# Kernel tuning notes

Measured on AMD Instinct MI355X. Metric: run time of the kernel, lower is better.

## Reference

```python
import jax, jax.numpy as jnp
import numpy as np

FRONT, END = 1, 2            # COMBINE_FRONT / COMBINE_END label values
BOS_ID, EOS_ID = 0, 1
BS, SLEN, D, H, L = 16, 256, 1024, 16, 2
N_POS = 512                  # N_MAX_POSITIONS


def setup_inputs():
    key = jax.random.key(0)
    ks = iter(jax.random.split(key, 80))
    nrm = lambda shape: jax.random.normal(next(ks), shape, dtype=jnp.float32) * 0.02
    inp = {}
    inp["encoded"] = jax.random.normal(next(ks), (BS, SLEN, D), dtype=jnp.float32)
    inp["lengths"] = jnp.full((BS,), SLEN, dtype=jnp.int32)  # assert slen == lengths.max()
    # deterministic valid word-span labels: [F,F,F,E,O,F,E,O] repeated -> words of 4 and 2 subwords
    pat = np.tile(np.array([1, 1, 1, 2, 0, 1, 2, 0], dtype=np.int32), SLEN // 8)
    inp["combine_labels"] = jnp.asarray(np.broadcast_to(pat, (BS, SLEN)).copy())
    inp["lang_id"] = 0
    inp["pos_emb"] = nrm((N_POS, D))
    inp["special_emb"] = nrm((3, D)).at[2].set(0.0)  # padding_idx=2 row zeroed
    for p in ("ctx", "wc"):
        for w in ("Wq", "Wk", "Wv", "Wo"):
            inp[p + "_" + w] = nrm((L, D, D))
        for b in ("bq", "bk", "bv", "bo", "b2", "be1", "be2"):
            inp[p + "_" + b] = jnp.zeros((L, D), dtype=jnp.float32)
        inp[p + "_W1"] = nrm((L, D, 4 * D))
        inp[p + "_b1"] = jnp.zeros((L, 4 * D), dtype=jnp.float32)
        inp[p + "_W2"] = nrm((L, 4 * D, D))
        inp[p + "_g1"] = jnp.ones((L, D), dtype=jnp.float32)
        inp[p + "_g2"] = jnp.ones((L, D), dtype=jnp.float32)
    return inp


def _ln(x, g, b):
    m = x.mean(-1, keepdims=True)
    v = ((x - m) ** 2).mean(-1, keepdims=True)
    return (x - m) / jnp.sqrt(v + 1e-5) * g + b


def _encoder(x, pad, P):
    # post-norm TransformerEncoder (torch default): attn -> add&LN -> relu-FFN -> add&LN
    Wq, Wk, Wv, Wo, bq, bk, bv, bo, W1, b1, W2, b2, g1, be1, g2, be2 = P
    B, S, Dm = x.shape
    hd = Dm // H
    scale = 1.0 / np.sqrt(hd)
    for i in range(Wq.shape[0]):
        q = (x @ Wq[i] + bq[i]).reshape(B, S, H, hd)
        k = (x @ Wk[i] + bk[i]).reshape(B, S, H, hd)
        v = (x @ Wv[i] + bv[i]).reshape(B, S, H, hd)
        s = jnp.einsum("bqhd,bkhd->bhqk", q, k) * scale
        s = jnp.where(pad[:, None, None, :], -1e9, s)  # src_key_padding_mask
        a = jax.nn.softmax(s, axis=-1)
        o = jnp.einsum("bhqk,bkhd->bqhd", a, v).reshape(B, S, Dm) @ Wo[i] + bo[i]
        x = _ln(x + o, g1[i], be1[i])
        h = jax.nn.relu(x @ W1[i] + b1[i]) @ W2[i] + b2[i]
        x = _ln(x + h, g2[i], be2[i])
    return x


def _word_inputs(encoded, combine_labels, special_emb):
    # vectorized replacement of the nested python-loop ragged span builder;
    # index math on the (concrete) labels in numpy, gathers/scatters in jnp.
    cl = np.asarray(combine_labels)
    f = cl == FRONT
    e = cl == END
    c = np.cumsum(f.astype(np.int64), axis=1)
    frontrun = c - np.maximum.accumulate(np.where(f, 0, c), axis=1)  # run of FRONTs ending here
    fr_prev = np.pad(frontrun[:, :-1], ((0, 0), (1, 0)))
    slot = np.where(f, frontrun, fr_prev + 1)  # 1-based slot inside word (slot 0 = BOS)
    e_flat = e.reshape(-1)
    wid = np.cumsum(e_flat) - e_flat  # word id = #ENDs strictly before, row-major order
    tok_idx = np.nonzero((f | e).reshape(-1))[0]
    w_tok = wid[tok_idx]
    s_tok = slot.reshape(-1)[tok_idx]
    wlen = fr_prev[e] + 3  # k subwords (fr_prev+1) + BOS + EOS
    n_word = wlen.shape[0]
    maxL = int(wlen.max())
    Dm = encoded.shape[-1]
    x = jnp.zeros((n_word, maxL, Dm), dtype=encoded.dtype)
    x = x.at[:, 0].set(special_emb[BOS_ID])
    x = x.at[np.arange(n_word), wlen - 1].set(special_emb[EOS_ID])  # eos at slot k+1
    x = x.at[w_tok, s_tok].set(encoded.reshape(-1, Dm)[tok_idx])
    return x, wlen


def _forward(encoded, lengths, combine_labels, pos_emb, special_emb, ctx, wc):
    S = encoded.shape[1]
    pad = jnp.asarray(np.arange(S)[None, :] >= np.asarray(lengths)[:, None])
    x = _encoder(encoded + pos_emb[:S][None], pad, ctx)          # another_encode
    winp, wlen = _word_inputs(x, combine_labels, special_emb)    # ragged gather, [n_word, maxL, D]
    maxL = winp.shape[1]
    wpad = jnp.asarray(np.arange(maxL)[None, :] >= wlen[:, None])
    y = _encoder(winp + pos_emb[:maxL][None], wpad, wc)          # word_encode
    return y[:, 0]  # position-0 (BOS) representation, [n_word, D]


def reference(encoded, lengths, combine_labels, lang_id, pos_emb, special_emb,
              ctx_Wq, ctx_Wk, ctx_Wv, ctx_Wo, ctx_bq, ctx_bk, ctx_bv, ctx_bo,
              ctx_W1, ctx_b1, ctx_W2, ctx_b2, ctx_g1, ctx_be1, ctx_g2, ctx_be2,
              wc_Wq, wc_Wk, wc_Wv, wc_Wo, wc_bq, wc_bk, wc_bv, wc_bo,
              wc_W1, wc_b1, wc_W2, wc_b2, wc_g1, wc_be1, wc_g2, wc_be2):
    ctx = (ctx_Wq, ctx_Wk, ctx_Wv, ctx_Wo, ctx_bq, ctx_bk, ctx_bv, ctx_bo,
           ctx_W1, ctx_b1, ctx_W2, ctx_b2, ctx_g1, ctx_be1, ctx_g2, ctx_be2)
    wc = (wc_Wq, wc_Wk, wc_Wv, wc_Wo, wc_bq, wc_bk, wc_bv, wc_bo,
          wc_W1, wc_b1, wc_W2, wc_b2, wc_g1, wc_be1, wc_g2, wc_be2)
    return _forward(encoded, lengths, combine_labels, pos_emb, special_emb, ctx, wc)
```

## Files before the change

### kernel.cpp

```cpp
#include <hip/hip_runtime.h>
#include <stdint.h>

typedef unsigned short u16;
typedef __attribute__((ext_vector_type(8))) short short8;
typedef __attribute__((ext_vector_type(4))) short short4v;
typedef __attribute__((ext_vector_type(4))) float f32x4;

#define DEV static __device__ __forceinline__

constexpr int B = 16, S = 256, D = 1024, H = 16, LYR = 2, FF = 4096;
constexpr int Mc = B * S;
constexpr int MAXL = 6;
constexpr int QKVS = 3 * D;

DEV u16 f2b(float f) {
  union { float f; uint32_t u; } a; a.f = f;
  uint32_t r = a.u + 0x7fffu + ((a.u >> 16) & 1u);
  return (u16)(r >> 16);
}
DEV float b2f(u16 b) {
  union { uint32_t u; float f; } a; a.u = ((uint32_t)b) << 16;
  return a.f;
}

DEV void glds16(const u16* g, u16* l) {
  __builtin_amdgcn_global_load_lds((const __attribute__((address_space(1))) void*)g,
                                   (__attribute__((address_space(3))) void*)l, 16, 0, 0);
}

struct TBatch {
  const float* src[6];
  u16* dst[6];
  int Kd[6];
  int Nd[6];
  int base[6];
};

__global__ __launch_bounds__(256) void transpose_batch(TBatch tb, int unused) {
  __shared__ float tile[32][33];
  const int bid = blockIdx.x;
  int wi = 0;
#pragma unroll
  for (int i = 1; i < 6; i++)
    if (bid >= tb.base[i]) wi = i;
  const float* __restrict__ W = tb.src[wi];
  u16* __restrict__ Wt = tb.dst[wi];
  const int K = tb.Kd[wi], N = tb.Nd[wi];
  const int local = bid - tb.base[wi];
  const int ntx = N >> 5;
  const int bn = (local % ntx) * 32, bk = (local / ntx) * 32;
  const int t = threadIdx.x, tx = t & 31, ty = t >> 5;
#pragma unroll
  for (int i = 0; i < 32; i += 8)
    tile[ty + i][tx] = W[(size_t)(bk + ty + i) * N + bn + tx];
  __syncthreads();
#pragma unroll
  for (int i = 0; i < 32; i += 8)
    Wt[(size_t)(bn + ty + i) * K + bk + tx] = f2b(tile[tx][ty + i]);
}


template <int PASSES>
DEV void stage_rows(const u16* P, int lda, int k0, u16* Dst, int t) {
#pragma unroll
  for (int p = 0; p < PASSES; p++)
    glds16(P + (size_t)(p * 32) * lda + k0, Dst + p * 2048 + t * 8);
}

DEV void compute_tile(const u16* Asb, const u16* Bsb, f32x4 (&acc)[4][8],
                      int wm, int wn, int li, int hi) {
#pragma unroll
  for (int ks = 0; ks < 2; ks++) {
    const int ch = ((((ks << 2) | hi) ^ (li & 7)) * 8);
    short8 af[4], bfr[8];
#pragma unroll
    for (int i = 0; i < 4; i++)
      af[i] = *(const short8*)&Asb[(wm + i * 16 + li) * 64 + ch];
#pragma unroll
    for (int j = 0; j < 8; j++)
      bfr[j] = *(const short8*)&Bsb[(wn + j * 16 + li) * 64 + ch];
#pragma unroll
    for (int i = 0; i < 4; i++)
#pragma unroll
      for (int j = 0; j < 8; j++)
        acc[i][j] = __builtin_amdgcn_mfma_f32_16x16x32_bf16(af[i], bfr[j], acc[i][j], 0, 0, 0);
  }
}

template <int EPI, bool SPLITB, bool SPLITK>
__global__ __launch_bounds__(256, 2) void gemm_bt(const u16* __restrict__ A,
                                                  const u16* __restrict__ Bt,
                                                  const float* __restrict__ bias0,
                                                  const float* __restrict__ bias1,
                                                  const float* __restrict__ bias2,
                                                  float* __restrict__ Cf, u16* __restrict__ Cb,
                                                  int M, int N, int K, int lda, int NB) {
  __shared__ u16 As[128 * 64];
  __shared__ u16 Bs[256 * 64];
  const int t = threadIdx.x, lane = t & 63, w = t >> 6;
  const int wm = (w >> 1) * 64, wn = (w & 1) * 128;
  const int nwg = gridDim.x;
  const int cpx = nwg >> 3;
  const int swz = (blockIdx.x & 7) * cpx + (blockIdx.x >> 3);
  int sblk = 0, rem = swz;
  if (SPLITK) {
    const int tps = nwg >> 1;
    sblk = (swz >= tps) ? 1 : 0;
    rem = swz - sblk * tps;
  }
  const int n0 = (rem % NB) * 256, m0 = (rem / NB) * 128;
  const int pr = t >> 3;
  const int scb = (((t & 7) ^ (pr & 7)) * 8);
  f32x4 acc[4][8] = {};
  const u16* Ap = A + (size_t)sblk * K + (size_t)(m0 + pr) * lda + scb;
  const u16* Bp = Bt + (size_t)sblk * K + (size_t)(n0 + pr) * lda + scb;
  const int li = lane & 15, hi = lane >> 4;

  for (int k0 = 0; k0 < K; k0 += 64) {
    stage_rows<4>(Ap, lda, k0, &As[0], t);
    stage_rows<8>(Bp, lda, k0, &Bs[0], t);
    __syncthreads();
    compute_tile(&As[0], &Bs[0], acc, wm, wn, li, hi);
    __syncthreads();
  }

  float* Cfs = Cf;
  if (SPLITK && EPI == 3) Cfs = Cf + (size_t)sblk * M * N;
  const int rg = hi * 4;
#pragma unroll
  for (int j = 0; j < 8; j++) {
    const int col = n0 + wn + j * 16 + li;
    float bv = 0.f;
    if (EPI != 3)
      bv = SPLITB ? (col < 1024 ? bias0 : col < 2048 ? bias1 : bias2)[col & 1023]
                  : bias0[col];
#pragma unroll
    for (int i = 0; i < 4; i++) {
      const int row0 = m0 + wm + i * 16 + rg;
#pragma unroll
      for (int r = 0; r < 4; r++) {
        float v = acc[i][j][r] + bv;
        if (EPI == 2) v = fmaxf(v, 0.f);
        if (EPI == 0 || EPI == 3) Cfs[(size_t)(row0 + r) * N + col] = v;
        else Cb[(size_t)(row0 + r) * N + col] = f2b(v);
      }
    }
  }
}

__global__ __launch_bounds__(256) void transpose_v(const u16* __restrict__ QKV,
                                                   u16* __restrict__ Vt) {
  const int kb = blockIdx.x, h = blockIdx.y, b = blockIdx.z;
  __shared__ u16 tile[64][72];
  const int t = threadIdx.x, lr = t >> 3, lc = (t & 7) * 8;
#pragma unroll
  for (int p = 0; p < 2; p++) {
    int r = lr + p * 32;
    *(short8*)&tile[r][lc] =
        *(const short8*)&QKV[(size_t)(b * 256 + kb * 64 + r) * QKVS + 2048 + h * 64 + lc];
  }
  __syncthreads();
#pragma unroll
  for (int p = 0; p < 2; p++) {
    int hd = lr + p * 32;
    short8 v8;
#pragma unroll
    for (int j = 0; j < 8; j++) v8[j] = (short)tile[lc + j][hd];
    *(short8*)&Vt[(size_t)((b * 16 + h) * 64 + hd) * 256 + kb * 64 + lc] = v8;
  }
}

__global__ __launch_bounds__(256) void attn_ctx(const u16* __restrict__ QKV,
                                                const u16* __restrict__ Vt,
                                                u16* __restrict__ AO,
                                                const int* __restrict__ lengths) {
  const int qt = blockIdx.x, h = blockIdx.y, b = blockIdx.z;
  __shared__ u16 Qs[64 * 64], Ks[64 * 64], Vs[64 * 64], Ps[64 * 64];
  const int t = threadIdx.x, lane = t & 63, w = t >> 6;
  const int len = lengths[b];
  const int lr = t >> 3, lc = (t & 7) * 8;
#pragma unroll
  for (int p = 0; p < 2; p++) {
    int r = lr + p * 32;
    *(short8*)&Qs[r * 64 + lc] =
        *(const short8*)&QKV[(size_t)(b * 256 + qt * 64 + r) * QKVS + h * 64 + lc];
  }
  const int li = lane & 15, kk = (lane >> 4) * 8, rg = (lane >> 4) * 4;
  float mrun[4], lrun[4];
  f32x4 oacc[4] = {};
#pragma unroll
  for (int r = 0; r < 4; r++) { mrun[r] = -1e30f; lrun[r] = 0.f; }

  for (int kt = 0; kt < 4; kt++) {
    __syncthreads();
#pragma unroll
    for (int p = 0; p < 2; p++) {
      int r = lr + p * 32;
      *(short8*)&Ks[r * 64 + lc] =
          *(const short8*)&QKV[(size_t)(b * 256 + kt * 64 + r) * QKVS + 1024 + h * 64 + lc];
      *(short8*)&Vs[r * 64 + lc] =
          *(const short8*)&Vt[(size_t)((b * 16 + h) * 64 + r) * 256 + kt * 64 + lc];
    }
    __syncthreads();
    f32x4 s[4] = {};
    short8 aq0 = *(const short8*)&Qs[(w * 16 + li) * 64 + kk];
    short8 aq1 = *(const short8*)&Qs[(w * 16 + li) * 64 + 32 + kk];
#pragma unroll
    for (int fn = 0; fn < 4; fn++) {
      short8 b0 = *(const short8*)&Ks[(fn * 16 + li) * 64 + kk];
      short8 b1 = *(const short8*)&Ks[(fn * 16 + li) * 64 + 32 + kk];
      s[fn] = __builtin_amdgcn_mfma_f32_16x16x32_bf16(aq0, b0, s[fn], 0, 0, 0);
      s[fn] = __builtin_amdgcn_mfma_f32_16x16x32_bf16(aq1, b1, s[fn], 0, 0, 0);
    }
    float pv[4][4];
#pragma unroll
    for (int r = 0; r < 4; r++) {
      float mx = -1e30f;
#pragma unroll
      for (int fn = 0; fn < 4; fn++) {
        int key = kt * 64 + fn * 16 + li;
        float v = (key < len) ? s[fn][r] * 0.125f : -1e30f;
        pv[fn][r] = v;
        mx = fmaxf(mx, v);
      }
#pragma unroll
      for (int d = 1; d < 16; d <<= 1) mx = fmaxf(mx, __shfl_xor(mx, d));
      float mnew = fmaxf(mrun[r], mx);
      float sf = __expf(mrun[r] - mnew);
      mrun[r] = mnew;
      float rs = 0.f;
#pragma unroll
      for (int fn = 0; fn < 4; fn++) {
        int key = kt * 64 + fn * 16 + li;
        float p = (key < len) ? __expf(pv[fn][r] - mnew) : 0.f;
        pv[fn][r] = p;
        rs += p;
      }
#pragma unroll
      for (int d = 1; d < 16; d <<= 1) rs += __shfl_xor(rs, d);
      lrun[r] = lrun[r] * sf + rs;
#pragma unroll
      for (int fn = 0; fn < 4; fn++) oacc[fn][r] *= sf;
    }
#pragma unroll
    for (int fn = 0; fn < 4; fn++)
#pragma unroll
      for (int r = 0; r < 4; r++)
        Ps[(w * 16 + rg + r) * 64 + fn * 16 + li] = f2b(pv[fn][r]);
#pragma unroll
    for (int ks = 0; ks < 2; ks++) {
      short8 ap = *(const short8*)&Ps[(w * 16 + li) * 64 + ks * 32 + kk];
#pragma unroll
      for (int fn = 0; fn < 4; fn++) {
        short8 bv = *(const short8*)&Vs[(fn * 16 + li) * 64 + ks * 32 + kk];
        oacc[fn] = __builtin_amdgcn_mfma_f32_16x16x32_bf16(ap, bv, oacc[fn], 0, 0, 0);
      }
    }
  }
#pragma unroll
  for (int r = 0; r < 4; r++) {
    float inv = 1.f / fmaxf(lrun[r], 1e-30f);
    int row = b * 256 + qt * 64 + w * 16 + rg + r;
#pragma unroll
    for (int fn = 0; fn < 4; fn++) {
      int col = h * 64 + fn * 16 + li;
      AO[(size_t)row * 1024 + col] = f2b(oacc[fn][r] * inv);
    }
  }
}

__global__ __launch_bounds__(256) void attn_word(const u16* __restrict__ QKV,
                                                 const int* __restrict__ wlen,
                                                 u16* __restrict__ AO, int NW) {
  const int idx = blockIdx.x * 256 + threadIdx.x;
  if (idx >= NW * 16 * MAXL) return;
  const int i = idx % MAXL, h = (idx / MAXL) % 16, wd = idx / (MAXL * 16);
  const int len = wlen[wd];
  const size_t rowb = (size_t)(wd * MAXL + i) * QKVS;
  float q[64];
#pragma unroll
  for (int d = 0; d < 64; d += 8) {
    short8 q8 = *(const short8*)&QKV[rowb + h * 64 + d];
#pragma unroll
    for (int e = 0; e < 8; e++) q[d + e] = b2f((u16)q8[e]);
  }
  float sc[MAXL];
  float mx = -1e30f;
  for (int j = 0; j < MAXL; j++) {
    if (j >= len) { sc[j] = -1e30f; continue; }
    const size_t koff = (size_t)(wd * MAXL + j) * QKVS + 1024 + h * 64;
    float dot = 0.f;
#pragma unroll
    for (int d = 0; d < 64; d += 8) {
      short8 k8 = *(const short8*)&QKV[koff + d];
#pragma unroll
      for (int e = 0; e < 8; e++) dot += q[d + e] * b2f((u16)k8[e]);
    }
    sc[j] = dot * 0.125f;
    mx = fmaxf(mx, sc[j]);
  }
  float p[MAXL], l = 0.f;
  for (int j = 0; j < MAXL; j++) {
    p[j] = (j < len) ? __expf(sc[j] - mx) : 0.f;
    l += p[j];
  }
  const float rl = 1.f / fmaxf(l, 1e-30f);
  for (int j = 0; j < MAXL; j++) p[j] *= rl;
#pragma unroll
  for (int d = 0; d < 64; d += 8) {
    float acc[8] = {};
    for (int j = 0; j < MAXL; j++) {
      if (j >= len) break;
      short8 v8 = *(const short8*)&QKV[(size_t)(wd * MAXL + j) * QKVS + 2048 + h * 64 + d];
#pragma unroll
      for (int e = 0; e < 8; e++) acc[e] += p[j] * b2f((u16)v8[e]);
    }
    short8 o8;
#pragma unroll
    for (int e = 0; e < 8; e++) o8[e] = (short)f2b(acc[e]);
    *(short8*)&AO[(size_t)(wd * MAXL + i) * 1024 + h * 64 + d] = o8;
  }
}

__global__ __launch_bounds__(256) void ln_resid2(const float* __restrict__ X,
                                                 const float* __restrict__ P0,
                                                 const float* __restrict__ P1,
                                                 const float* __restrict__ bias,
                                                 const float* __restrict__ g,
                                                 const float* __restrict__ be,
                                                 float* __restrict__ Xo, u16* __restrict__ Xb) {
  const int row = blockIdx.x, t = threadIdx.x;
  const size_t base = (size_t)row * 1024 + t * 4;
  float4 x4 = *(const float4*)&X[base];
  float4 p0 = *(const float4*)&P0[base];
  float4 p1 = *(const float4*)&P1[base];
  float4 bb = *(const float4*)&bias[t * 4];
  float v[4] = { x4.x + p0.x + p1.x + bb.x, x4.y + p0.y + p1.y + bb.y,
                 x4.z + p0.z + p1.z + bb.z, x4.w + p0.w + p1.w + bb.w };
  float s = v[0] + v[1] + v[2] + v[3];
  float q = v[0] * v[0] + v[1] * v[1] + v[2] * v[2] + v[3] * v[3];
#pragma unroll
  for (int d = 1; d < 64; d <<= 1) { s += __shfl_xor(s, d); q += __shfl_xor(q, d); }
  __shared__ float ss[4], qq[4];
  if ((t & 63) == 0) { ss[t >> 6] = s; qq[t >> 6] = q; }
  __syncthreads();
  s = ss[0] + ss[1] + ss[2] + ss[3];
  q = qq[0] + qq[1] + qq[2] + qq[3];
  const float mean = s * (1.f / 1024.f);
  const float var = q * (1.f / 1024.f) - mean * mean;
  const float rstd = rsqrtf(var + 1e-5f);
  float4 gv = *(const float4*)&g[t * 4];
  float4 bv = *(const float4*)&be[t * 4];
  float y[4];
  y[0] = (v[0] - mean) * rstd * gv.x + bv.x;
  y[1] = (v[1] - mean) * rstd * gv.y + bv.y;
  y[2] = (v[2] - mean) * rstd * gv.z + bv.z;
  y[3] = (v[3] - mean) * rstd * gv.w + bv.w;
  *(float4*)&Xo[base] = make_float4(y[0], y[1], y[2], y[3]);
  short4v o = { (short)f2b(y[0]), (short)f2b(y[1]), (short)f2b(y[2]), (short)f2b(y[3]) };
  *(short4v*)&Xb[base] = o;
}

__global__ __launch_bounds__(256) void posadd(const float* __restrict__ enc,
                                              const float* __restrict__ pos,
                                              float* __restrict__ X, u16* __restrict__ Xb) {
  const int row = blockIdx.x, t = threadIdx.x;
  const int sp = row & 255;
  const size_t base = (size_t)row * 1024 + t * 4;
  float4 e = *(const float4*)&enc[base];
  float4 p = *(const float4*)&pos[(size_t)sp * 1024 + t * 4];
  float y[4] = { e.x + p.x, e.y + p.y, e.z + p.z, e.w + p.w };
  *(float4*)&X[base] = make_float4(y[0], y[1], y[2], y[3]);
  short4v o = { (short)f2b(y[0]), (short)f2b(y[1]), (short)f2b(y[2]), (short)f2b(y[3]) };
  *(short4v*)&Xb[base] = o;
}

__global__ void scan_words(const int* __restrict__ labels, int* __restrict__ t2w,
                           int* __restrict__ t2s, int* __restrict__ wlen) {
  __shared__ int rowEnds[16], rowBase[16];
  const int t = threadIdx.x;
  if (t < 16) {
    int c = 0;
    for (int s = 0; s < 256; s++) c += (labels[t * 256 + s] == 2);
    rowEnds[t] = c;
  }
  __syncthreads();
  if (t == 0) {
    int acc = 0;
    for (int b2 = 0; b2 < 16; b2++) { rowBase[b2] = acc; acc += rowEnds[b2]; }
  }
  __syncthreads();
  if (t < 16) {
    int wc = rowBase[t], fr = 0;
    for (int s = 0; s < 256; s++) {
      const int tok = t * 256 + s, lb = labels[tok];
      if (lb == 1) { fr++; t2w[tok] = wc; t2s[tok] = fr; }
      else if (lb == 2) { t2w[tok] = wc; t2s[tok] = fr + 1; wlen[wc] = fr + 3; wc++; fr = 0; }
      else { t2w[tok] = -1; t2s[tok] = 0; fr = 0; }
    }
  }
}

__global__ __launch_bounds__(256) void build_winp(const float* __restrict__ pos,
                                                  const float* __restrict__ spec,
                                                  const int* __restrict__ wlen,
                                                  float* __restrict__ XW) {
  const int row = blockIdx.x;
  const int wd = row / MAXL, sl = row % MAXL;
  const int len = wlen[wd];
  const int t = threadIdx.x;
  const size_t cb = t * 4;
  float4 p = *(const float4*)&pos[(size_t)sl * 1024 + cb];
  float4 e = make_float4(0.f, 0.f, 0.f, 0.f);
  if (sl == 0) e = *(const float4*)&spec[cb];
  else if (sl == len - 1) e = *(const float4*)&spec[1024 + cb];
  *(float4*)&XW[(size_t)row * 1024 + cb] =
      make_float4(p.x + e.x, p.y + e.y, p.z + e.z, p.w + e.w);
}

__global__ __launch_bounds__(256) void scatter_tokens(const float* __restrict__ Xc,
                                                      const int* __restrict__ t2w,
                                                      const int* __restrict__ t2s,
                                                      float* __restrict__ XW) {
  const int tok = blockIdx.x;
  const int wd = t2w[tok];
  if (wd < 0) return;
  const int row = wd * MAXL + t2s[tok];
  const size_t cb = threadIdx.x * 4;
  float4 a = *(const float4*)&Xc[(size_t)tok * 1024 + cb];
  float* dst = &XW[(size_t)row * 1024 + cb];
  float4 b2 = *(const float4*)dst;
  *(float4*)dst = make_float4(a.x + b2.x, a.y + b2.y, a.z + b2.z, a.w + b2.w);
}

__global__ __launch_bounds__(256) void to_bf16_k(const float* __restrict__ X,
                                                 u16* __restrict__ Xb) {
  const size_t base = (size_t)blockIdx.x * 1024 + threadIdx.x * 4;
  float4 v = *(const float4*)&X[base];
  short4v o = { (short)f2b(v.x), (short)f2b(v.y), (short)f2b(v.z), (short)f2b(v.w) };
  *(short4v*)&Xb[base] = o;
}

__global__ __launch_bounds__(256) void gather_out(const float* __restrict__ XW,
                                                  float* __restrict__ out) {
  const int wd = blockIdx.x;
  const size_t cb = threadIdx.x * 4;
  *(float4*)&out[(size_t)wd * 1024 + cb] =
      *(const float4*)&XW[(size_t)(wd * MAXL) * 1024 + cb];
}

extern "C" void kernel_launch(void* const* d_in, const int* in_sizes, int n_in,
                              void* d_out, int out_size, void* d_ws, size_t ws_size,
                              hipStream_t stream) {
  const float* encoded = (const float*)d_in[0];
  const int* lengths = (const int*)d_in[1];
  const int* labels = (const int*)d_in[2];
  const float* pos = (const float*)d_in[4];
  const float* spec = (const float*)d_in[5];
  const float* W[2][16];
  for (int p = 0; p < 2; p++)
    for (int i = 0; i < 16; i++) W[p][i] = (const float*)d_in[6 + p * 16 + i];

  const int NW = out_size / D;
  const int Mw = NW * MAXL;

  char* wp = (char*)d_ws;
  size_t off = 0;
  auto alloc = [&](size_t bytes) {
    void* r = wp + off;
    off += (bytes + 255) & ~(size_t)255;
    return r;
  };
  float* x_ctx = (float*)alloc((size_t)Mc * D * 4);
  float* x_word = (float*)alloc((size_t)Mw * D * 4);
  u16* xb = (u16*)alloc((size_t)Mw * D * 2);
  u16* wtQKV = (u16*)alloc((size_t)3 * D * D * 2);
  u16* wtO = (u16*)alloc((size_t)D * D * 2);
  u16* wtW1 = (u16*)alloc((size_t)D * FF * 2);
  u16* wtW2 = (u16*)alloc((size_t)D * FF * 2);
  char* uni = (char*)alloc((size_t)Mw * FF * 2);
  u16* QKV = (u16*)uni;
  u16* Vt = (u16*)(uni + ((size_t)40 << 20));
  u16* hb = (u16*)uni;
  u16* AOb = (u16*)alloc((size_t)Mw * D * 2);
  float* tmp = (float*)alloc((size_t)2 * Mw * D * 4);
  int* t2w = (int*)alloc((size_t)Mc * 4);
  int* t2s = (int*)alloc((size_t)Mc * 4);
  int* wlen = (int*)alloc((size_t)NW * 4);
  (void)ws_size; (void)in_sizes; (void)n_in;

  posadd<<<Mc, 256, 0, stream>>>(encoded, pos, x_ctx, xb);

  auto run_encoder = [&](int p, float* X, int M, bool is_ctx) {
    for (int l = 0; l < LYR; l++) {
      const size_t oDD = (size_t)l * D * D, oDF = (size_t)l * D * FF;
      TBatch tb;
      tb.src[0] = W[p][0] + oDD; tb.dst[0] = wtQKV;               tb.Kd[0] = D;  tb.Nd[0] = D;
      tb.src[1] = W[p][1] + oDD; tb.dst[1] = wtQKV + (size_t)D * D;   tb.Kd[1] = D;  tb.Nd[1] = D;
      tb.src[2] = W[p][2] + oDD; tb.dst[2] = wtQKV + (size_t)2 * D * D; tb.Kd[2] = D; tb.Nd[2] = D;
      tb.src[3] = W[p][3] + oDD; tb.dst[3] = wtO;                 tb.Kd[3] = D;  tb.Nd[3] = D;
      tb.src[4] = W[p][11] + oDF; tb.dst[4] = wtW1;               tb.Kd[4] = D;  tb.Nd[4] = FF;
      tb.src[5] = W[p][13] + oDF; tb.dst[5] = wtW2;               tb.Kd[5] = FF; tb.Nd[5] = D;
      int base = 0;
      for (int i = 0; i < 6; i++) {
        tb.base[i] = base;
        base += (tb.Kd[i] / 32) * (tb.Nd[i] / 32);
      }
      transpose_batch<<<base, 256, 0, stream>>>(tb, 0);

      gemm_bt<1, true, false><<<(3 * D / 256) * (M / 128), 256, 0, stream>>>(
          xb, wtQKV, W[p][4] + (size_t)l * D, W[p][5] + (size_t)l * D,
          W[p][6] + (size_t)l * D, nullptr, QKV, M, 3 * D, D, D, 3 * D / 256);
      if (is_ctx) {
        transpose_v<<<dim3(4, H, B), 256, 0, stream>>>(QKV, Vt);
        attn_ctx<<<dim3(4, H, B), 256, 0, stream>>>(QKV, Vt, AOb, lengths);
      } else {
        attn_word<<<(NW * H * MAXL + 255) / 256, 256, 0, stream>>>(QKV, wlen, AOb, NW);
      }
      gemm_bt<3, false, true><<<2 * (D / 256) * (M / 128), 256, 0, stream>>>(
          AOb, wtO, nullptr, nullptr, nullptr, tmp, nullptr, M, D, 512, D, D / 256);
      ln_resid2<<<M, 256, 0, stream>>>(X, tmp, tmp + (size_t)M * D, W[p][7] + (size_t)l * D,
                                       W[p][14] + (size_t)l * D, W[p][9] + (size_t)l * D, X, xb);
      gemm_bt<2, false, false><<<(FF / 256) * (M / 128), 256, 0, stream>>>(
          xb, wtW1, W[p][12] + (size_t)l * FF, nullptr, nullptr, nullptr, hb, M, FF, D, D,
          FF / 256);
      gemm_bt<3, false, true><<<2 * (D / 256) * (M / 128), 256, 0, stream>>>(
          hb, wtW2, nullptr, nullptr, nullptr, tmp, nullptr, M, D, 2048, FF, D / 256);
      ln_resid2<<<M, 256, 0, stream>>>(X, tmp, tmp + (size_t)M * D, W[p][8] + (size_t)l * D,
                                       W[p][15] + (size_t)l * D, W[p][10] + (size_t)l * D, X, xb);
    }
  };

  run_encoder(0, x_ctx, Mc, true);

  scan_words<<<1, 64, 0, stream>>>(labels, t2w, t2s, wlen);
  build_winp<<<Mw, 256, 0, stream>>>(pos, spec, wlen, x_word);
  scatter_tokens<<<Mc, 256, 0, stream>>>(x_ctx, t2w, t2s, x_word);
  to_bf16_k<<<Mw, 256, 0, stream>>>(x_word, xb);

  run_encoder(1, x_word, Mw, false);

  gather_out<<<NW, 256, 0, stream>>>(x_word, (float*)d_out);
}
```

Measured before the change: 1.042 ms.

## Widen weight transpose tiles, store split-K partials as bf16, tune attention softmax

The weight transpose kernel now uses 64x64 tiles with float4 loads and 16-byte bf16 stores. Split-K GEMM partials are written as bf16 instead of fp32 and read back as bf16 in the residual+LayerNorm kernel, halving that traffic. The context attention kernel adds a no-mask fast path with lazy max rescaling (rescale only when the max grows by more than 8). It also raises wave priority around its MFMA blocks. Storing partial sums in bf16 loses precision before they are summed.

```diff
diff --git a/kernel.cpp b/kernel.cpp
--- a/kernel.cpp
+++ b/kernel.cpp
@@ -37,7 +37,7 @@
 };
 
 __global__ __launch_bounds__(256) void transpose_batch(TBatch tb, int unused) {
-  __shared__ float tile[32][33];
+  __shared__ float tile[64][65];
   const int bid = blockIdx.x;
   int wi = 0;
 #pragma unroll
@@ -47,16 +47,25 @@
   u16* __restrict__ Wt = tb.dst[wi];
   const int K = tb.Kd[wi], N = tb.Nd[wi];
   const int local = bid - tb.base[wi];
-  const int ntx = N >> 5;
-  const int bn = (local % ntx) * 32, bk = (local / ntx) * 32;
-  const int t = threadIdx.x, tx = t & 31, ty = t >> 5;
-#pragma unroll
-  for (int i = 0; i < 32; i += 8)
-    tile[ty + i][tx] = W[(size_t)(bk + ty + i) * N + bn + tx];
+  const int ntx = N >> 6;
+  const int bn = (local % ntx) * 64, bk = (local / ntx) * 64;
+  const int t = threadIdx.x;
+  const int lr = t >> 2, lc = (t & 3) * 16;
+#pragma unroll
+  for (int q = 0; q < 4; q++) {
+    float4 v = *(const float4*)&W[(size_t)(bk + lr) * N + bn + lc + q * 4];
+    *(float4*)&tile[lr][lc + q * 4] = v;
+  }
   __syncthreads();
-#pragma unroll
-  for (int i = 0; i < 32; i += 8)
-    Wt[(size_t)(bn + ty + i) * K + bk + tx] = f2b(tile[tx][ty + i]);
+  const int k0 = (t & 7) * 8;
+#pragma unroll
+  for (int p = 0; p < 2; p++) {
+    const int n = (t >> 3) + p * 32;
+    short8 o;
+#pragma unroll
+    for (int j = 0; j < 8; j++) o[j] = (short)f2b(tile[k0 + j][n]);
+    *(short8*)&Wt[(size_t)(bn + n) * K + bk + k0] = o;
+  }
 }
 
 
@@ -124,8 +133,8 @@
     __syncthreads();
   }
 
-  float* Cfs = Cf;
-  if (SPLITK && EPI == 3) Cfs = Cf + (size_t)sblk * M * N;
+  u16* Cbs = Cb;
+  if (SPLITK && EPI == 3) Cbs = Cb + (size_t)sblk * M * N;
   const int rg = hi * 4;
 #pragma unroll
   for (int j = 0; j < 8; j++) {
@@ -141,8 +150,8 @@
       for (int r = 0; r < 4; r++) {
         float v = acc[i][j][r] + bv;
         if (EPI == 2) v = fmaxf(v, 0.f);
-        if (EPI == 0 || EPI == 3) Cfs[(size_t)(row0 + r) * N + col] = v;
-        else Cb[(size_t)(row0 + r) * N + col] = f2b(v);
+        if (EPI == 0) Cf[(size_t)(row0 + r) * N + col] = v;
+        else Cbs[(size_t)(row0 + r) * N + col] = f2b(v);
       }
     }
   }
@@ -178,6 +187,7 @@
   __shared__ u16 Qs[64 * 64], Ks[64 * 64], Vs[64 * 64], Ps[64 * 64];
   const int t = threadIdx.x, lane = t & 63, w = t >> 6;
   const int len = lengths[b];
+  const bool full = (len >= 256);
   const int lr = t >> 3, lc = (t & 7) * 8;
 #pragma unroll
   for (int p = 0; p < 2; p++) {
@@ -205,6 +215,7 @@
     f32x4 s[4] = {};
     short8 aq0 = *(const short8*)&Qs[(w * 16 + li) * 64 + kk];
     short8 aq1 = *(const short8*)&Qs[(w * 16 + li) * 64 + 32 + kk];
+    __builtin_amdgcn_s_setprio(1);
 #pragma unroll
     for (int fn = 0; fn < 4; fn++) {
       short8 b0 = *(const short8*)&Ks[(fn * 16 + li) * 64 + kk];
@@ -212,41 +223,75 @@
       s[fn] = __builtin_amdgcn_mfma_f32_16x16x32_bf16(aq0, b0, s[fn], 0, 0, 0);
       s[fn] = __builtin_amdgcn_mfma_f32_16x16x32_bf16(aq1, b1, s[fn], 0, 0, 0);
     }
+    __builtin_amdgcn_s_setprio(0);
     float pv[4][4];
-#pragma unroll
-    for (int r = 0; r < 4; r++) {
-      float mx = -1e30f;
-#pragma unroll
-      for (int fn = 0; fn < 4; fn++) {
-        int key = kt * 64 + fn * 16 + li;
-        float v = (key < len) ? s[fn][r] * 0.125f : -1e30f;
-        pv[fn][r] = v;
-        mx = fmaxf(mx, v);
+    if (full) {
+#pragma unroll
+      for (int r = 0; r < 4; r++) {
+        float mx = -1e30f;
+#pragma unroll
+        for (int fn = 0; fn < 4; fn++) {
+          float v = s[fn][r] * 0.125f;
+          pv[fn][r] = v;
+          mx = fmaxf(mx, v);
+        }
+#pragma unroll
+        for (int d = 1; d < 16; d <<= 1) mx = fmaxf(mx, __shfl_xor(mx, d));
+        if (mx > mrun[r] + 8.f) {
+          float sf = __expf(mrun[r] - mx);
+          mrun[r] = mx;
+          lrun[r] *= sf;
+#pragma unroll
+          for (int fn = 0; fn < 4; fn++) oacc[fn][r] *= sf;
+        }
+        float rs = 0.f;
+#pragma unroll
+        for (int fn = 0; fn < 4; fn++) {
+          float p = __expf(pv[fn][r] - mrun[r]);
+          pv[fn][r] = p;
+          rs += p;
+        }
+#pragma unroll
+        for (int d = 1; d < 16; d <<= 1) rs += __shfl_xor(rs, d);
+        lrun[r] += rs;
       }
-#pragma unroll
-      for (int d = 1; d < 16; d <<= 1) mx = fmaxf(mx, __shfl_xor(mx, d));
-      float mnew = fmaxf(mrun[r], mx);
-      float sf = __expf(mrun[r] - mnew);
-      mrun[r] = mnew;
-      float rs = 0.f;
-#pragma unroll
-      for (int fn = 0; fn < 4; fn++) {
-        int key = kt * 64 + fn * 16 + li;
-        float p = (key < len) ? __expf(pv[fn][r] - mnew) : 0.f;
-        pv[fn][r] = p;
-        rs += p;
+    } else {
+#pragma unroll
+      for (int r = 0; r < 4; r++) {
+        float mx = -1e30f;
+#pragma unroll
+        for (int fn = 0; fn < 4; fn++) {
+          int key = kt * 64 + fn * 16 + li;
+          float v = (key < len) ? s[fn][r] * 0.125f : -1e30f;
+          pv[fn][r] = v;
+          mx = fmaxf(mx, v);
+        }
+#pragma unroll
+        for (int d = 1; d < 16; d <<= 1) mx = fmaxf(mx, __shfl_xor(mx, d));
+        float mnew = fmaxf(mrun[r], mx);
+        float sf = __expf(mrun[r] - mnew);
+        mrun[r] = mnew;
+        float rs = 0.f;
+#pragma unroll
+        for (int fn = 0; fn < 4; fn++) {
+          int key = kt * 64 + fn * 16 + li;
+          float p = (key < len) ? __expf(pv[fn][r] - mnew) : 0.f;
+          pv[fn][r] = p;
+          rs += p;
+        }
+#pragma unroll
+        for (int d = 1; d < 16; d <<= 1) rs += __shfl_xor(rs, d);
+        lrun[r] = lrun[r] * sf + rs;
+#pragma unroll
+        for (int fn = 0; fn < 4; fn++) oacc[fn][r] *= sf;
       }
-#pragma unroll
-      for (int d = 1; d < 16; d <<= 1) rs += __shfl_xor(rs, d);
-      lrun[r] = lrun[r] * sf + rs;
-#pragma unroll
-      for (int fn = 0; fn < 4; fn++) oacc[fn][r] *= sf;
     }
 #pragma unroll
     for (int fn = 0; fn < 4; fn++)
 #pragma unroll
       for (int r = 0; r < 4; r++)
         Ps[(w * 16 + rg + r) * 64 + fn * 16 + li] = f2b(pv[fn][r]);
+    __builtin_amdgcn_s_setprio(1);
 #pragma unroll
     for (int ks = 0; ks < 2; ks++) {
       short8 ap = *(const short8*)&Ps[(w * 16 + li) * 64 + ks * 32 + kk];
@@ -256,6 +301,7 @@
         oacc[fn] = __builtin_amdgcn_mfma_f32_16x16x32_bf16(ap, bv, oacc[fn], 0, 0, 0);
       }
     }
+    __builtin_amdgcn_s_setprio(0);
   }
 #pragma unroll
   for (int r = 0; r < 4; r++) {
@@ -323,8 +369,8 @@
 }
 
 __global__ __launch_bounds__(256) void ln_resid2(const float* __restrict__ X,
-                                                 const float* __restrict__ P0,
-                                                 const float* __restrict__ P1,
+                                                 const u16* __restrict__ P0,
+                                                 const u16* __restrict__ P1,
                                                  const float* __restrict__ bias,
                                                  const float* __restrict__ g,
                                                  const float* __restrict__ be,
@@ -332,11 +378,14 @@
   const int row = blockIdx.x, t = threadIdx.x;
   const size_t base = (size_t)row * 1024 + t * 4;
   float4 x4 = *(const float4*)&X[base];
-  float4 p0 = *(const float4*)&P0[base];
-  float4 p1 = *(const float4*)&P1[base];
+  short4v p0 = *(const short4v*)&P0[base];
+  short4v p1 = *(const short4v*)&P1[base];
   float4 bb = *(const float4*)&bias[t * 4];
-  float v[4] = { x4.x + p0.x + p1.x + bb.x, x4.y + p0.y + p1.y + bb.y,
-                 x4.z + p0.z + p1.z + bb.z, x4.w + p0.w + p1.w + bb.w };
+  float v[4];
+  v[0] = x4.x + b2f((u16)p0[0]) + b2f((u16)p1[0]) + bb.x;
+  v[1] = x4.y + b2f((u16)p0[1]) + b2f((u16)p1[1]) + bb.y;
+  v[2] = x4.z + b2f((u16)p0[2]) + b2f((u16)p1[2]) + bb.z;
+  v[3] = x4.w + b2f((u16)p0[3]) + b2f((u16)p1[3]) + bb.w;
   float s = v[0] + v[1] + v[2] + v[3];
   float q = v[0] * v[0] + v[1] * v[1] + v[2] * v[2] + v[3] * v[3];
 #pragma unroll
@@ -483,7 +532,7 @@
   u16* Vt = (u16*)(uni + ((size_t)40 << 20));
   u16* hb = (u16*)uni;
   u16* AOb = (u16*)alloc((size_t)Mw * D * 2);
-  float* tmp = (float*)alloc((size_t)2 * Mw * D * 4);
+  u16* tmpb = (u16*)alloc((size_t)2 * Mw * D * 2);
   int* t2w = (int*)alloc((size_t)Mc * 4);
   int* t2s = (int*)alloc((size_t)Mc * 4);
   int* wlen = (int*)alloc((size_t)NW * 4);
@@ -504,7 +553,7 @@
       int base = 0;
       for (int i = 0; i < 6; i++) {
         tb.base[i] = base;
-        base += (tb.Kd[i] / 32) * (tb.Nd[i] / 32);
+        base += (tb.Kd[i] / 64) * (tb.Nd[i] / 64);
       }
       transpose_batch<<<base, 256, 0, stream>>>(tb, 0);
 
@@ -518,15 +567,15 @@
         attn_word<<<(NW * H * MAXL + 255) / 256, 256, 0, stream>>>(QKV, wlen, AOb, NW);
       }
       gemm_bt<3, false, true><<<2 * (D / 256) * (M / 128), 256, 0, stream>>>(
-          AOb, wtO, nullptr, nullptr, nullptr, tmp, nullptr, M, D, 512, D, D / 256);
-      ln_resid2<<<M, 256, 0, stream>>>(X, tmp, tmp + (size_t)M * D, W[p][7] + (size_t)l * D,
+          AOb, wtO, nullptr, nullptr, nullptr, nullptr, tmpb, M, D, 512, D, D / 256);
+      ln_resid2<<<M, 256, 0, stream>>>(X, tmpb, tmpb + (size_t)M * D, W[p][7] + (size_t)l * D,
                                        W[p][14] + (size_t)l * D, W[p][9] + (size_t)l * D, X, xb);
       gemm_bt<2, false, false><<<(FF / 256) * (M / 128), 256, 0, stream>>>(
           xb, wtW1, W[p][12] + (size_t)l * FF, nullptr, nullptr, nullptr, hb, M, FF, D, D,
           FF / 256);
       gemm_bt<3, false, true><<<2 * (D / 256) * (M / 128), 256, 0, stream>>>(
-          hb, wtW2, nullptr, nullptr, nullptr, tmp, nullptr, M, D, 2048, FF, D / 256);
-      ln_resid2<<<M, 256, 0, stream>>>(X, tmp, tmp + (size_t)M * D, W[p][8] + (size_t)l * D,
+          hb, wtW2, nullptr, nullptr, nullptr, nullptr, tmpb, M, D, 2048, FF, D / 256);
+      ln_resid2<<<M, 256, 0, stream>>>(X, tmpb, tmpb + (size_t)M * D, W[p][8] + (size_t)l * D,
                                        W[p][15] + (size_t)l * D, W[p][10] + (size_t)l * D, X, xb);
     }
   };
```

Result: faster. 1.013 ms (-2.8%).
